# Optimization experiments

Hardware: AMD Instinct MI355X
Metric: run time of the kernel (lower is better)

The kernel has to match this reference:

```python
import jax, jax.numpy as jnp
import numpy as np
from jax.ops import segment_sum, segment_max

N, E, F, HID, HEADS, OUT, G = 50000, 800000, 128, 64, 2, 128, 50
EPS = 1e-5


def setup_inputs() -> dict:
    key = jax.random.key(0)
    ks = iter(jax.random.split(key, 80))
    def p(*shape):
        return jax.random.normal(next(ks), shape, jnp.float32) * 0.1
    inp = {}
    inp['x'] = jax.random.normal(next(ks), (N, F), jnp.float32)
    inp['edge_index'] = jax.random.randint(next(ks), (2, E), 0, N)
    inp['batch'] = jnp.repeat(jnp.arange(G), N // G)
    dims = [(F, HID), (HID, HID), (HID, OUT)]
    for i, (a, b) in enumerate(dims):
        inp[f'gcn_W{i}'] = p(a, b); inp[f'gcn_b{i}'] = jnp.zeros((b,), jnp.float32)
    for i in range(2):
        inp[f'gcn_bn_g{i}'] = jnp.ones((HID,), jnp.float32); inp[f'gcn_bn_b{i}'] = jnp.zeros((HID,), jnp.float32)
    gat_dims = [(F, HEADS, HID), (HEADS * HID, HEADS, HID), (HEADS * HID, 1, OUT)]
    for i, (a, h, c) in enumerate(gat_dims):
        inp[f'gat_W{i}'] = p(a, h * c)
        inp[f'gat_as{i}'] = p(h, c)
        inp[f'gat_ad{i}'] = p(h, c)
        inp[f'gat_b{i}'] = jnp.zeros((h * c if i < 2 else c,), jnp.float32)
    for i in range(2):
        inp[f'gat_bn_g{i}'] = jnp.ones((HEADS * HID,), jnp.float32); inp[f'gat_bn_b{i}'] = jnp.zeros((HEADS * HID,), jnp.float32)
    for i, (a, b) in enumerate(dims):
        inp[f'sage_Wl{i}'] = p(a, b); inp[f'sage_Wr{i}'] = p(a, b); inp[f'sage_b{i}'] = jnp.zeros((b,), jnp.float32)
    for i in range(2):
        inp[f'sage_bn_g{i}'] = jnp.ones((HID,), jnp.float32); inp[f'sage_bn_b{i}'] = jnp.zeros((HID,), jnp.float32)
    inp['fus_W'] = p(3 * OUT, OUT); inp['fus_b'] = jnp.zeros((OUT,), jnp.float32)
    return inp


def _bn(x, g, b):
    m = x.mean(0)
    v = x.var(0)
    return (x - m) * jax.lax.rsqrt(v + EPS) * g + b


def _pool(x, batch):
    s = segment_sum(x, batch, num_segments=G)
    c = segment_sum(jnp.ones((x.shape[0], 1), x.dtype), batch, num_segments=G)
    return s / jnp.maximum(c, 1.0)


def _with_self_loops(src, dst):
    loop = jnp.arange(N)
    return jnp.concatenate([src, loop]), jnp.concatenate([dst, loop])


def _gcn_conv(x, W, b, src, dst):
    # PyG GCNConv: linear, add self loops, symmetric D^-1/2 normalization, scatter-add at dst
    h = x @ W
    srcf, dstf = _with_self_loops(src, dst)
    deg = segment_sum(jnp.ones(srcf.shape[0], x.dtype), dstf, num_segments=N)
    dis = jnp.where(deg > 0, jax.lax.rsqrt(jnp.maximum(deg, 1.0)), 0.0)
    norm = dis[srcf] * dis[dstf]
    return segment_sum(h[srcf] * norm[:, None], dstf, num_segments=N) + b


def _gat_conv(x, W, a_s, a_d, b, src, dst, concat):
    # PyG GATConv: per-head additive attention, leaky_relu(0.2), softmax over incoming edges
    Hh, C = a_s.shape
    h = (x @ W).reshape(N, Hh, C)
    al_src = (h * a_s).sum(-1)  # [N,H]
    al_dst = (h * a_d).sum(-1)  # [N,H]
    srcf, dstf = _with_self_loops(src, dst)
    e = jax.nn.leaky_relu(al_src[srcf] + al_dst[dstf], 0.2)  # [E+N,H]
    m = segment_max(e, dstf, num_segments=N)
    ex = jnp.exp(e - m[dstf])
    denom = segment_sum(ex, dstf, num_segments=N)
    alpha = ex / (denom[dstf] + 1e-16)
    out = segment_sum(h[srcf] * alpha[:, :, None], dstf, num_segments=N)  # [N,H,C]
    out = out.reshape(N, Hh * C) if concat else out.mean(1)
    return out + b


def _sage_conv(x, Wl, Wr, b, src, dst):
    # PyG SAGEConv(mean): lin_l(mean of neighbors) + lin_r(x)
    s = segment_sum(x[src], dst, num_segments=N)
    cnt = segment_sum(jnp.ones((E, 1), x.dtype), dst, num_segments=N)
    mean = s / jnp.maximum(cnt, 1.0)
    return mean @ Wl + x @ Wr + b


def _forward(x, edge_index, batch,
             gcn_W0, gcn_b0, gcn_W1, gcn_b1, gcn_W2, gcn_b2,
             gcn_bn_g0, gcn_bn_b0, gcn_bn_g1, gcn_bn_b1,
             gat_W0, gat_as0, gat_ad0, gat_b0,
             gat_W1, gat_as1, gat_ad1, gat_b1,
             gat_W2, gat_as2, gat_ad2, gat_b2,
             gat_bn_g0, gat_bn_b0, gat_bn_g1, gat_bn_b1,
             sage_Wl0, sage_Wr0, sage_b0,
             sage_Wl1, sage_Wr1, sage_b1,
             sage_Wl2, sage_Wr2, sage_b2,
             sage_bn_g0, sage_bn_b0, sage_bn_g1, sage_bn_b1,
             fus_W, fus_b):
    src, dst = edge_index[0], edge_index[1]
    # GCN branch
    h = jax.nn.relu(_bn(_gcn_conv(x, gcn_W0, gcn_b0, src, dst), gcn_bn_g0, gcn_bn_b0))
    h = jax.nn.relu(_bn(_gcn_conv(h, gcn_W1, gcn_b1, src, dst), gcn_bn_g1, gcn_bn_b1))
    h = _gcn_conv(h, gcn_W2, gcn_b2, src, dst)
    gcn_out = _pool(h, batch)
    # GAT branch (2 heads concat, final single head)
    h = jax.nn.elu(_bn(_gat_conv(x, gat_W0, gat_as0, gat_ad0, gat_b0, src, dst, True), gat_bn_g0, gat_bn_b0))
    h = jax.nn.elu(_bn(_gat_conv(h, gat_W1, gat_as1, gat_ad1, gat_b1, src, dst, True), gat_bn_g1, gat_bn_b1))
    h = _gat_conv(h, gat_W2, gat_as2, gat_ad2, gat_b2, src, dst, False)
    gat_out = _pool(h, batch)
    # SAGE branch (mean aggregation)
    h = jax.nn.relu(_bn(_sage_conv(x, sage_Wl0, sage_Wr0, sage_b0, src, dst), sage_bn_g0, sage_bn_b0))
    h = jax.nn.relu(_bn(_sage_conv(h, sage_Wl1, sage_Wr1, sage_b1, src, dst), sage_bn_g1, sage_bn_b1))
    h = _sage_conv(h, sage_Wl2, sage_Wr2, sage_b2, src, dst)
    sage_out = _pool(h, batch)
    combined = jnp.concatenate([gcn_out, gat_out, sage_out], axis=-1)  # [G, 3*OUT]
    return combined @ fus_W + fus_b


def reference(x, edge_index, batch,
              gcn_W0, gcn_b0, gcn_W1, gcn_b1, gcn_W2, gcn_b2,
              gcn_bn_g0, gcn_bn_b0, gcn_bn_g1, gcn_bn_b1,
              gat_W0, gat_as0, gat_ad0, gat_b0,
              gat_W1, gat_as1, gat_ad1, gat_b1,
              gat_W2, gat_as2, gat_ad2, gat_b2,
              gat_bn_g0, gat_bn_b0, gat_bn_g1, gat_bn_b1,
              sage_Wl0, sage_Wr0, sage_b0,
              sage_Wl1, sage_Wr1, sage_b1,
              sage_Wl2, sage_Wr2, sage_b2,
              sage_bn_g0, sage_bn_b0, sage_bn_g1, sage_bn_b1,
              fus_W, fus_b):
    return _forward(x, edge_index, batch,
                    gcn_W0, gcn_b0, gcn_W1, gcn_b1, gcn_W2, gcn_b2,
                    gcn_bn_g0, gcn_bn_b0, gcn_bn_g1, gcn_bn_b1,
                    gat_W0, gat_as0, gat_ad0, gat_b0,
                    gat_W1, gat_as1, gat_ad1, gat_b1,
                    gat_W2, gat_as2, gat_ad2, gat_b2,
                    gat_bn_g0, gat_bn_b0, gat_bn_g1, gat_bn_b1,
                    sage_Wl0, sage_Wr0, sage_b0,
                    sage_Wl1, sage_Wr1, sage_b1,
                    sage_Wl2, sage_Wr2, sage_b2,
                    sage_bn_g0, sage_bn_b0, sage_bn_g1, sage_bn_b1,
                    fus_W, fus_b)
```

## Files before the change

### kernel.cpp

```cpp
#include <hip/hip_runtime.h>

#define NN 50000
#define NE 800000
#define NG 50
#define NB 196

static constexpr float BN_EPS = 1e-5f;

typedef __attribute__((ext_vector_type(8))) short  bf16x8;
typedef __attribute__((ext_vector_type(8))) unsigned short u16x8;
typedef __attribute__((ext_vector_type(4))) float  f32x4;

__device__ __forceinline__ float bf2f(unsigned short u) {
    return __uint_as_float(((unsigned)u) << 16);
}
__device__ __forceinline__ unsigned short f2bf(float f) {
    unsigned u = __float_as_uint(f);
    unsigned r = (u + 0x7fffu + ((u >> 16) & 1u)) >> 16;
    return (unsigned short)r;
}

__global__ void k_indeg(const int* __restrict__ dst, int* __restrict__ indeg) {
    int e = blockIdx.x * 256 + threadIdx.x;
    if (e < NE) atomicAdd(&indeg[dst[e]], 1);
}

__global__ void k_scan1(const int* __restrict__ cnt, int* __restrict__ rowstart,
                        int* __restrict__ bsum, float* __restrict__ dis) {
    int i = blockIdx.x * 256 + threadIdx.x;
    int lane = threadIdx.x & 63, wv = threadIdx.x >> 6;
    int v = (i < NN) ? cnt[i] : 0;
    if (i < NN) dis[i] = rsqrtf((float)v + 1.0f);
    int s = v;
#pragma unroll
    for (int d = 1; d < 64; d <<= 1) {
        int t = __shfl_up(s, d);
        if (lane >= d) s += t;
    }
    __shared__ int wtot[4];
    if (lane == 63) wtot[wv] = s;
    __syncthreads();
    int woff = 0;
    for (int w = 0; w < wv; ++w) woff += wtot[w];
    if (i < NN) rowstart[i] = woff + s - v;
    if (threadIdx.x == 255) bsum[blockIdx.x] = woff + s;
}

__global__ void k_scan2(const int* __restrict__ bsum, int* __restrict__ boff) {
    int lane = threadIdx.x & 63, wv = threadIdx.x >> 6;
    int v = (threadIdx.x < NB) ? bsum[threadIdx.x] : 0;
    int s = v;
#pragma unroll
    for (int d = 1; d < 64; d <<= 1) {
        int t = __shfl_up(s, d);
        if (lane >= d) s += t;
    }
    __shared__ int wtot[4];
    if (lane == 63) wtot[wv] = s;
    __syncthreads();
    int woff = 0;
    for (int w = 0; w < wv; ++w) woff += wtot[w];
    if (threadIdx.x < NB) boff[threadIdx.x] = woff + s - v;
}

__global__ void k_scan3(int* __restrict__ rowstart, const int* __restrict__ boff,
                        int* __restrict__ cursor) {
    int i = blockIdx.x * 256 + threadIdx.x;
    if (i < NN) {
        int v = rowstart[i] + boff[blockIdx.x];
        rowstart[i] = v;
        cursor[i] = v;
    }
    if (i == 0) rowstart[NN] = NE;
}

__global__ void k_fill(const int* __restrict__ src, const int* __restrict__ dst,
                       const float* __restrict__ dis, int* __restrict__ cursor,
                       int2* __restrict__ pair) {
    int e = blockIdx.x * 256 + threadIdx.x;
    if (e < NE) {
        int s = src[e];
        int pos = atomicAdd(&cursor[dst[e]], 1);
        pair[pos] = make_int2(s, __float_as_int(dis[s]));
    }
}

__global__ void k_count(const int* __restrict__ batch, float* __restrict__ cntG) {
    __shared__ int hist[NG];
    for (int i = threadIdx.x; i < NG; i += 256) hist[i] = 0;
    __syncthreads();
    for (int n = blockIdx.x * 256 + threadIdx.x; n < NN; n += gridDim.x * 256)
        atomicAdd(&hist[batch[n]], 1);
    __syncthreads();
    for (int i = threadIdx.x; i < NG; i += 256)
        if (hist[i]) atomicAdd(&cntG[i], (float)hist[i]);
}

struct WDesc { const float* s; unsigned short* d; int fin; int fout; };
struct WTable { WDesc w[12]; };

__global__ void k_convw(WTable t) {
    WDesc wd = t.w[blockIdx.x];
    int total = wd.fin * wd.fout;
    for (int i = threadIdx.x; i < total; i += 256) {
        int c = i / wd.fin, k = i % wd.fin;
        wd.d[i] = f2bf(wd.s[(size_t)k * wd.fout + c]);
    }
}

__global__ __launch_bounds__(256) void k_mm0(
        const float* __restrict__ X, const unsigned short* __restrict__ Wf,
        const float* __restrict__ as_, const float* __restrict__ ad_,
        float* __restrict__ alsrc, float* __restrict__ aldst,
        unsigned short* __restrict__ outGCN, unsigned short* __restrict__ outGAT,
        unsigned short* __restrict__ outSL, unsigned short* __restrict__ outSR) {
    constexpr int FIN = 128, NCT = 20;
    int wave = threadIdx.x >> 6, lane = threadIdx.x & 63;
    int rowbase = (blockIdx.x * 4 + wave) * 16;
    if (rowbase >= NN) return;
    int lr = lane & 15, lg = lane >> 4;
    int arow = rowbase + lr;
    f32x4 acc[NCT] = {};
    const float* xp = X + (size_t)arow * FIN + lg * 8;
#pragma unroll
    for (int k0 = 0; k0 < FIN; k0 += 32) {
        float4 v0 = *(const float4*)(xp + k0);
        float4 v1 = *(const float4*)(xp + k0 + 4);
        u16x8 au;
        au[0] = f2bf(v0.x); au[1] = f2bf(v0.y); au[2] = f2bf(v0.z); au[3] = f2bf(v0.w);
        au[4] = f2bf(v1.x); au[5] = f2bf(v1.y); au[6] = f2bf(v1.z); au[7] = f2bf(v1.w);
        bf16x8 a1 = *(bf16x8*)&au;
#pragma unroll
        for (int ct = 0; ct < NCT; ++ct) {
            int wcol = ct * 16 + lr;
            bf16x8 b1 = *(const bf16x8*)(Wf + (size_t)wcol * FIN + k0 + lg * 8);
            acc[ct] = __builtin_amdgcn_mfma_f32_16x16x32_bf16(a1, b1, acc[ct], 0, 0, 0);
        }
    }
    {
        float ps[2][4] = {}, pd[2][4] = {};
#pragma unroll
        for (int ct = 4; ct < 12; ++ct) {
            int hh = (ct >= 8) ? 1 : 0;
            int colg = ct * 16 + lr - 64;
            float cs = as_[colg], cd = ad_[colg];
#pragma unroll
            for (int j = 0; j < 4; ++j) {
                ps[hh][j] += acc[ct][j] * cs;
                pd[hh][j] += acc[ct][j] * cd;
            }
        }
#pragma unroll
        for (int m = 1; m < 16; m <<= 1)
#pragma unroll
            for (int hh = 0; hh < 2; ++hh)
#pragma unroll
                for (int j = 0; j < 4; ++j) {
                    ps[hh][j] += __shfl_xor(ps[hh][j], m);
                    pd[hh][j] += __shfl_xor(pd[hh][j], m);
                }
        if (lr == 0) {
#pragma unroll
            for (int j = 0; j < 4; ++j) {
                int row = rowbase + lg * 4 + j;
#pragma unroll
                for (int hh = 0; hh < 2; ++hh) {
                    alsrc[(size_t)row * 2 + hh] = ps[hh][j];
                    aldst[(size_t)row * 2 + hh] = pd[hh][j];
                }
            }
        }
    }
#pragma unroll
    for (int ct = 0; ct < NCT; ++ct) {
        int col = ct * 16 + lr;
#pragma unroll
        for (int j = 0; j < 4; ++j) {
            int row = rowbase + lg * 4 + j;
            unsigned short v = f2bf(acc[ct][j]);
            if (ct < 4)       outGCN[(size_t)row * 64 + col] = v;
            else if (ct < 12) outGAT[(size_t)row * 128 + (col - 64)] = v;
            else if (ct < 16) outSL[(size_t)row * 64 + (col - 192)] = v;
            else              outSR[(size_t)row * 64 + (col - 256)] = v;
        }
    }
}

template <int FIN, int FOUT, bool DUAL, bool BIAS, int BNACT, int ALH>
__global__ __launch_bounds__(256) void k_mm(
        const unsigned short* __restrict__ A1, const unsigned short* __restrict__ W1t,
        const unsigned short* __restrict__ A2, const unsigned short* __restrict__ W2t,
        const float* __restrict__ bias,
        const float* __restrict__ bns, const float* __restrict__ bng, const float* __restrict__ bnb,
        const float* __restrict__ as_, const float* __restrict__ ad_,
        float* __restrict__ alsrc, float* __restrict__ aldst,
        unsigned short* __restrict__ out) {
    constexpr int NCT = FOUT / 16;
    int wave = threadIdx.x >> 6, lane = threadIdx.x & 63;
    int rowbase = (blockIdx.x * 4 + wave) * 16;
    if (rowbase >= NN) return;
    int lr = lane & 15, lg = lane >> 4;
    int arow = rowbase + lr;
    f32x4 acc[NCT] = {};
    const unsigned short* a1p = A1 + (size_t)arow * FIN + lg * 8;
    const unsigned short* a2p = DUAL ? (A2 + (size_t)arow * FIN + lg * 8) : nullptr;
#pragma unroll
    for (int k0 = 0; k0 < FIN; k0 += 32) {
        bf16x8 a1;
        if (BNACT == 0) {
            a1 = *(const bf16x8*)(a1p + k0);
        } else {
            u16x8 araw = *(const u16x8*)(a1p + k0);
            u16x8 atx;
#pragma unroll
            for (int j = 0; j < 8; ++j) {
                int f = k0 + lg * 8 + j;
                float mean = bns[f] * (1.0f / NN);
                float var = bns[FIN + f] * (1.0f / NN) - mean * mean;
                float rstd = rsqrtf(var + BN_EPS);
                float val = (bf2f(araw[j]) - mean) * rstd * bng[f] + bnb[f];
                if (BNACT == 1) val = fmaxf(val, 0.f);
                if (BNACT == 2) val = (val > 0.f) ? val : (__expf(val) - 1.0f);
                atx[j] = f2bf(val);
            }
            a1 = *(bf16x8*)&atx;
        }
        bf16x8 a2v = {};
        if (DUAL) a2v = *(const bf16x8*)(a2p + k0);
#pragma unroll
        for (int ct = 0; ct < NCT; ++ct) {
            int wcol = ct * 16 + lr;
            bf16x8 b1 = *(const bf16x8*)(W1t + (size_t)wcol * FIN + k0 + lg * 8);
            acc[ct] = __builtin_amdgcn_mfma_f32_16x16x32_bf16(a1, b1, acc[ct], 0, 0, 0);
            if (DUAL) {
                bf16x8 b2 = *(const bf16x8*)(W2t + (size_t)wcol * FIN + k0 + lg * 8);
                acc[ct] = __builtin_amdgcn_mfma_f32_16x16x32_bf16(a2v, b2, acc[ct], 0, 0, 0);
            }
        }
    }
    if (ALH > 0) {
        constexpr int NH = (ALH > 0) ? ALH : 1;
        float ps[NH][4] = {}, pd[NH][4] = {};
#pragma unroll
        for (int ct = 0; ct < NCT; ++ct) {
            int hh = (ALH == 2 && ct >= NCT / 2) ? 1 : 0;
            int col = ct * 16 + lr;
            float cs = as_[col], cd = ad_[col];
#pragma unroll
            for (int j = 0; j < 4; ++j) {
                ps[hh][j] += acc[ct][j] * cs;
                pd[hh][j] += acc[ct][j] * cd;
            }
        }
#pragma unroll
        for (int m = 1; m < 16; m <<= 1)
#pragma unroll
            for (int hh = 0; hh < NH; ++hh)
#pragma unroll
                for (int j = 0; j < 4; ++j) {
                    ps[hh][j] += __shfl_xor(ps[hh][j], m);
                    pd[hh][j] += __shfl_xor(pd[hh][j], m);
                }
        if (lr == 0) {
#pragma unroll
            for (int j = 0; j < 4; ++j) {
                int row = rowbase + lg * 4 + j;
#pragma unroll
                for (int hh = 0; hh < NH; ++hh) {
                    alsrc[(size_t)row * ALH + hh] = ps[hh][j];
                    aldst[(size_t)row * ALH + hh] = pd[hh][j];
                }
            }
        }
    }
#pragma unroll
    for (int ct = 0; ct < NCT; ++ct) {
        int col = ct * 16 + lr;
        float bv = BIAS ? bias[col] : 0.f;
#pragma unroll
        for (int j = 0; j < 4; ++j) {
            int row = rowbase + lg * 4 + j;
            out[(size_t)row * FOUT + col] = f2bf(acc[ct][j] + bv);
        }
    }
}

template <int F, bool BIAS>
__global__ __launch_bounds__(256) void k_gcn_agg(
        const int* __restrict__ rowstart, const int2* __restrict__ pair,
        const float* __restrict__ dis, const unsigned short* __restrict__ h,
        const float* __restrict__ bias, unsigned short* __restrict__ out) {
    constexpr int LPE = F / 8;
    constexpr int EPW = 64 / LPE;
    int wave = threadIdx.x >> 6, lane = threadIdx.x & 63;
    int n = blockIdx.x * 4 + wave;
    if (n >= NN) return;
    int r0 = rowstart[n], r1 = rowstart[n + 1];
    float dn = dis[n];
    int fl = lane % LPE, eg = lane / LPE;
    int f0 = fl * 8;
    float acc[8] = {};
    if (eg == 0) {
        u16x8 hv = *(const u16x8*)&h[(size_t)n * F + f0];
        float c = dn * dn;
#pragma unroll
        for (int j = 0; j < 8; ++j) acc[j] = c * bf2f(hv[j]);
    }
#pragma unroll 4
    for (int e = r0 + eg; e < r1; e += EPW) {
        int2 p = pair[e];
        float c = __int_as_float(p.y) * dn;
        u16x8 hs = *(const u16x8*)&h[(size_t)p.x * F + f0];
#pragma unroll
        for (int jj = 0; jj < 8; ++jj) acc[jj] += c * bf2f(hs[jj]);
    }
#pragma unroll
    for (int off = LPE; off < 64; off <<= 1)
#pragma unroll
        for (int jj = 0; jj < 8; ++jj) acc[jj] += __shfl_xor(acc[jj], off);
    if (eg == 0) {
        u16x8 o;
#pragma unroll
        for (int jj = 0; jj < 8; ++jj) {
            float v = acc[jj];
            if (BIAS) v += bias[f0 + jj];
            o[jj] = f2bf(v);
        }
        *(u16x8*)&out[(size_t)n * F + f0] = o;
    }
}

template <int F>
__global__ __launch_bounds__(256) void k_sage_agg(
        const int* __restrict__ rowstart, const int2* __restrict__ pair,
        const unsigned short* __restrict__ h, unsigned short* __restrict__ out) {
    constexpr int LPE = F / 8;
    constexpr int EPW = 64 / LPE;
    int wave = threadIdx.x >> 6, lane = threadIdx.x & 63;
    int n = blockIdx.x * 4 + wave;
    if (n >= NN) return;
    int r0 = rowstart[n], r1 = rowstart[n + 1];
    int fl = lane % LPE, eg = lane / LPE;
    int f0 = fl * 8;
    float acc[8] = {};
#pragma unroll 4
    for (int e = r0 + eg; e < r1; e += EPW) {
        int2 p = pair[e];
        u16x8 hs = *(const u16x8*)&h[(size_t)p.x * F + f0];
#pragma unroll
        for (int jj = 0; jj < 8; ++jj) acc[jj] += bf2f(hs[jj]);
    }
#pragma unroll
    for (int off = LPE; off < 64; off <<= 1)
#pragma unroll
        for (int jj = 0; jj < 8; ++jj) acc[jj] += __shfl_xor(acc[jj], off);
    if (eg == 0) {
        float inv = 1.0f / fmaxf((float)(r1 - r0), 1.0f);
        u16x8 o;
#pragma unroll
        for (int jj = 0; jj < 8; ++jj) o[jj] = f2bf(acc[jj] * inv);
        *(u16x8*)&out[(size_t)n * F + f0] = o;
    }
}

template <int H, int C, bool BIAS>
__global__ __launch_bounds__(256) void k_gat_agg(
        const int* __restrict__ rowstart, const int2* __restrict__ pair,
        const float* __restrict__ alsrc, const float* __restrict__ aldst,
        const unsigned short* __restrict__ h, const float* __restrict__ bias,
        unsigned short* __restrict__ out) {
    constexpr int HC = H * C;
    constexpr int LPE = HC / 8;
    constexpr int EPW = 64 / LPE;
    constexpr int HL = C / 8;
    int wave = threadIdx.x >> 6, lane = threadIdx.x & 63;
    int n = blockIdx.x * 4 + wave;
    if (n >= NN) return;
    int r0 = rowstart[n], r1 = rowstart[n + 1];
    int fl = lane % LPE, eg = lane / LPE;
    int f0 = fl * 8;
    int hh = (H > 1) ? (fl / HL) : 0;
    float adn = aldst[n * H + hh];
    float t = alsrc[n * H + hh] + adn;
    float ws = __expf((t >= 0.f) ? t : 0.2f * t);
    float acc[8] = {};
    float dsum = 0.f;
    if (eg == 0) {
        u16x8 hv = *(const u16x8*)&h[(size_t)n * HC + f0];
#pragma unroll
        for (int j = 0; j < 8; ++j) acc[j] = ws * bf2f(hv[j]);
    }
#pragma unroll 4
    for (int e = r0 + eg; e < r1; e += EPW) {
        int s = pair[e].x;
        float v = alsrc[(size_t)s * H + hh] + adn;
        v = (v >= 0.f) ? v : 0.2f * v;
        float w = __expf(v);
        dsum += w;
        u16x8 hs = *(const u16x8*)&h[(size_t)s * HC + f0];
#pragma unroll
        for (int jj = 0; jj < 8; ++jj) acc[jj] += w * bf2f(hs[jj]);
    }
    if (H > 1) {
#pragma unroll
        for (int off = 1; off < HL; off <<= 1) dsum += __shfl_xor(dsum, off);
#pragma unroll
        for (int off = LPE; off < 64; off <<= 1) dsum += __shfl_xor(dsum, off);
    } else {
#pragma unroll
        for (int off = 1; off < 64; off <<= 1) dsum += __shfl_xor(dsum, off);
    }
    float den = ws + dsum * (1.0f / HL);
    float dinv = 1.0f / (den + 1e-16f);
#pragma unroll
    for (int off = LPE; off < 64; off <<= 1)
#pragma unroll
        for (int jj = 0; jj < 8; ++jj) acc[jj] += __shfl_xor(acc[jj], off);
    if (eg == 0) {
        u16x8 o;
#pragma unroll
        for (int jj = 0; jj < 8; ++jj) {
            float v = acc[jj] * dinv;
            if (BIAS) v += bias[f0 + jj];
            o[jj] = f2bf(v);
        }
        *(u16x8*)&out[(size_t)n * HC + f0] = o;
    }
}

template <int F, bool TWO>
__global__ void k_bn_stats(const unsigned short* __restrict__ x,
                           const unsigned short* __restrict__ y,
                           float* __restrict__ sums) {
    constexpr int TPR = F / 8;
    constexpr int RPB = 256 / TPR;
    __shared__ float lsum[F], lsq[F];
    for (int i = threadIdx.x; i < F; i += 256) { lsum[i] = 0.f; lsq[i] = 0.f; }
    __syncthreads();
    int fl = threadIdx.x % TPR, rl = threadIdx.x / TPR;
    int f0 = fl * 8;
    float s[8] = {}, s2[8] = {};
    for (int n = blockIdx.x * RPB + rl; n < NN; n += gridDim.x * RPB) {
        u16x8 v = *(const u16x8*)&x[(size_t)n * F + f0];
        u16x8 w = {};
        if (TWO) w = *(const u16x8*)&y[(size_t)n * F + f0];
#pragma unroll
        for (int j = 0; j < 8; ++j) {
            float f = bf2f(v[j]);
            if (TWO) f += bf2f(w[j]);
            s[j] += f; s2[j] += f * f;
        }
    }
#pragma unroll
    for (int off = TPR; off < 64; off <<= 1)
#pragma unroll
        for (int j = 0; j < 8; ++j) { s[j] += __shfl_xor(s[j], off); s2[j] += __shfl_xor(s2[j], off); }
    if ((threadIdx.x & 63) < TPR) {
#pragma unroll
        for (int j = 0; j < 8; ++j) {
            atomicAdd(&lsum[f0 + j], s[j]);
            atomicAdd(&lsq[f0 + j], s2[j]);
        }
    }
    __syncthreads();
    for (int i = threadIdx.x; i < F; i += 256) {
        atomicAdd(&sums[i], lsum[i]);
        atomicAdd(&sums[F + i], lsq[i]);
    }
}

template <int F, int ACT, bool TWO>
__global__ void k_bn_apply(const unsigned short* __restrict__ x,
                           const unsigned short* __restrict__ y,
                           const float* __restrict__ sums,
                           const float* __restrict__ gamma, const float* __restrict__ beta,
                           unsigned short* __restrict__ out) {
    int idx = blockIdx.x * 256 + threadIdx.x;
    if (idx >= NN * F / 8) return;
    int f0 = (idx % (F / 8)) * 8;
    u16x8 v = *(const u16x8*)&x[(size_t)idx * 8];
    u16x8 w = {};
    if (TWO) w = *(const u16x8*)&y[(size_t)idx * 8];
    u16x8 o;
#pragma unroll
    for (int j = 0; j < 8; ++j) {
        int f = f0 + j;
        float mean = sums[f] * (1.0f / NN);
        float var = sums[F + f] * (1.0f / NN) - mean * mean;
        float rstd = rsqrtf(var + BN_EPS);
        float raw = bf2f(v[j]);
        if (TWO) raw += bf2f(w[j]);
        float val = (raw - mean) * rstd * gamma[f] + beta[f];
        if (ACT == 1) val = fmaxf(val, 0.f);
        if (ACT == 2) val = (val > 0.f) ? val : (__expf(val) - 1.0f);
        o[j] = f2bf(val);
    }
    *(u16x8*)&out[(size_t)idx * 8] = o;
}

__global__ void k_pool(const unsigned short* __restrict__ x, const int* __restrict__ batch,
                       float* __restrict__ pooled, int off) {
    int f = threadIdx.x & 127;
    int half = threadIdx.x >> 7;
    int nend = min(NN, (int)(blockIdx.x + 1) * 128);
    float acc = 0.f; int gcur = -1;
    for (int n = blockIdx.x * 128 + half; n < nend; n += 2) {
        int g = batch[n];
        if (g != gcur) {
            if (gcur >= 0) atomicAdd(&pooled[(size_t)gcur * 384 + off + f], acc);
            gcur = g; acc = 0.f;
        }
        acc += bf2f(x[(size_t)n * 128 + f]);
    }
    if (gcur >= 0) atomicAdd(&pooled[(size_t)gcur * 384 + off + f], acc);
}

__global__ void k_fusion(const float* __restrict__ pooled, const float* __restrict__ cntG,
                         const float* __restrict__ W, const float* __restrict__ b,
                         float* __restrict__ out) {
    int idx = blockIdx.x * 256 + threadIdx.x;
    if (idx >= NG * 128) return;
    int g = idx / 128, o = idx % 128;
    float inv = 1.0f / fmaxf(cntG[g], 1.0f);
    float acc = b[o];
#pragma unroll 4
    for (int k = 0; k < 384; ++k)
        acc += pooled[g * 384 + k] * inv * W[k * 128 + o];
    out[idx] = acc;
}

static inline int grid1(long long n) { return (int)((n + 255) / 256); }

extern "C" void kernel_launch(void* const* d_in, const int* in_sizes, int n_in,
                              void* d_out, int out_size, void* d_ws, size_t ws_size,
                              hipStream_t stream) {
    const float* x       = (const float*)d_in[0];
    const int*   ei      = (const int*)d_in[1];
    const int*   batch   = (const int*)d_in[2];
    const float* gcn_W0  = (const float*)d_in[3];
    const float* gcn_W1  = (const float*)d_in[5];
    const float* gcn_W2  = (const float*)d_in[7];
    const float* gcn_b2  = (const float*)d_in[8];
    const float* gcn_g0  = (const float*)d_in[9];
    const float* gcn_bb0 = (const float*)d_in[10];
    const float* gcn_g1  = (const float*)d_in[11];
    const float* gcn_bb1 = (const float*)d_in[12];
    const float* gat_W0  = (const float*)d_in[13];
    const float* gat_as0 = (const float*)d_in[14];
    const float* gat_ad0 = (const float*)d_in[15];
    const float* gat_W1  = (const float*)d_in[17];
    const float* gat_as1 = (const float*)d_in[18];
    const float* gat_ad1 = (const float*)d_in[19];
    const float* gat_W2  = (const float*)d_in[21];
    const float* gat_as2 = (const float*)d_in[22];
    const float* gat_ad2 = (const float*)d_in[23];
    const float* gat_b2  = (const float*)d_in[24];
    const float* gat_g0  = (const float*)d_in[25];
    const float* gat_bb0 = (const float*)d_in[26];
    const float* gat_g1  = (const float*)d_in[27];
    const float* gat_bb1 = (const float*)d_in[28];
    const float* sage_Wl0 = (const float*)d_in[29];
    const float* sage_Wr0 = (const float*)d_in[30];
    const float* sage_Wl1 = (const float*)d_in[32];
    const float* sage_Wr1 = (const float*)d_in[33];
    const float* sage_Wl2 = (const float*)d_in[35];
    const float* sage_Wr2 = (const float*)d_in[36];
    const float* sage_b2  = (const float*)d_in[37];
    const float* sage_g0  = (const float*)d_in[38];
    const float* sage_bb0 = (const float*)d_in[39];
    const float* sage_g1  = (const float*)d_in[40];
    const float* sage_bb1 = (const float*)d_in[41];
    const float* fus_W    = (const float*)d_in[42];
    const float* fus_b    = (const float*)d_in[43];

    const int* src = ei;
    const int* dst = ei + NE;

    float* ws = (float*)d_ws;
    size_t off = 0;
    auto alloc = [&](size_t n) { float* p = ws + off; off += (n + 3) & ~(size_t)3; return p; };
    unsigned short* bufA  = (unsigned short*)alloc((size_t)NN * 64);
    unsigned short* bufB  = (unsigned short*)alloc((size_t)NN * 64);
    unsigned short* bufC  = (unsigned short*)alloc((size_t)NN * 64);
    unsigned short* bufD  = (unsigned short*)alloc((size_t)NN * 64);
    unsigned short* wt    = (unsigned short*)alloc(110592 / 2);
    int*   indeg    = (int*)alloc(NN);
    int*   rowstart = (int*)alloc(NN + 1);
    int*   cursor   = (int*)alloc(NN);
    int2*  pair     = (int2*)alloc((size_t)NE * 2);
    int*   bsum     = (int*)alloc(NB);
    int*   boff     = (int*)alloc(NB);
    float* dis   = alloc(NN);
    float* alsrc = alloc((size_t)NN * 2);
    float* aldst = alloc((size_t)NN * 2);
    float* bnsum = alloc(6 * 256 + NG * 384 + NG);
    float* pooled = bnsum + 6 * 256;
    float* cntG   = pooled + NG * 384;
    (void)ws_size; (void)n_in; (void)in_sizes; (void)out_size;

    unsigned short* sl0 = bufD;
    unsigned short* sr0 = bufD + (size_t)NN * 64;

    unsigned short* wf       = wt;
    unsigned short* gcn_W1t  = wf + 40960;
    unsigned short* gcn_W2t  = gcn_W1t + 4096;
    unsigned short* gat_W1t  = gcn_W2t + 8192;
    unsigned short* gat_W2t  = gat_W1t + 16384;
    unsigned short* sage_Wl1t = gat_W2t + 16384;
    unsigned short* sage_Wr1t = sage_Wl1t + 4096;
    unsigned short* sage_Wl2t = sage_Wr1t + 4096;
    unsigned short* sage_Wr2t = sage_Wl2t + 8192;

    const int gAgg = NN / 4;
    const int gMM  = (NN + 63) / 64;

    hipMemsetAsync(indeg, 0, NN * 4, stream);
    hipMemsetAsync(bnsum, 0, (6 * 256 + NG * 384 + NG) * 4, stream);
    k_indeg<<<grid1(NE), 256, 0, stream>>>(dst, indeg);
    k_scan1<<<NB, 256, 0, stream>>>(indeg, rowstart, bsum, dis);
    k_scan2<<<1, 256, 0, stream>>>(bsum, boff);
    k_scan3<<<NB, 256, 0, stream>>>(rowstart, boff, cursor);
    k_fill<<<grid1(NE), 256, 0, stream>>>(src, dst, dis, cursor, pair);
    k_count<<<128, 256, 0, stream>>>(batch, cntG);
    WTable wtab = {{
        { gcn_W0, wf, 128, 64 }, { gat_W0, wf + 64 * 128, 128, 128 },
        { sage_Wl0, wf + 192 * 128, 128, 64 }, { sage_Wr0, wf + 256 * 128, 128, 64 },
        { gcn_W1, gcn_W1t, 64, 64 }, { gcn_W2, gcn_W2t, 64, 128 },
        { gat_W1, gat_W1t, 128, 128 }, { gat_W2, gat_W2t, 128, 128 },
        { sage_Wl1, sage_Wl1t, 64, 64 }, { sage_Wr1, sage_Wr1t, 64, 64 },
        { sage_Wl2, sage_Wl2t, 64, 128 }, { sage_Wr2, sage_Wr2t, 64, 128 },
    }};
    k_convw<<<12, 256, 0, stream>>>(wtab);

    k_mm0<<<gMM, 256, 0, stream>>>(x, wf, gat_as0, gat_ad0, alsrc, aldst,
                                   bufA, bufB, sl0, sr0);

    k_gcn_agg<64, false><<<gAgg, 256, 0, stream>>>(rowstart, pair, dis, bufA, nullptr, bufC);
    k_bn_stats<64, false><<<250, 256, 0, stream>>>(bufC, nullptr, bnsum + 0 * 256);
    k_mm<64, 64, false, false, 1, 0><<<gMM, 256, 0, stream>>>(
        bufC, gcn_W1t, nullptr, nullptr, nullptr,
        bnsum + 0 * 256, gcn_g0, gcn_bb0, nullptr, nullptr, nullptr, nullptr, bufA);
    k_gcn_agg<64, false><<<gAgg, 256, 0, stream>>>(rowstart, pair, dis, bufA, nullptr, bufC);
    k_bn_stats<64, false><<<250, 256, 0, stream>>>(bufC, nullptr, bnsum + 1 * 256);
    k_bn_apply<64, 1, false><<<grid1(NN * 8), 256, 0, stream>>>(
        bufC, nullptr, bnsum + 1 * 256, gcn_g1, gcn_bb1, bufA);
    k_gcn_agg<64, false><<<gAgg, 256, 0, stream>>>(rowstart, pair, dis, bufA, nullptr, bufC);
    k_mm<64, 128, false, true, 0, 0><<<gMM, 256, 0, stream>>>(
        bufC, gcn_W2t, nullptr, nullptr, gcn_b2,
        nullptr, nullptr, nullptr, nullptr, nullptr, nullptr, nullptr, bufA);
    k_pool<<<(NN + 127) / 128, 256, 0, stream>>>(bufA, batch, pooled, 0);

    k_gat_agg<2, 64, false><<<gAgg, 256, 0, stream>>>(rowstart, pair, alsrc, aldst, bufB, nullptr, bufC);
    k_bn_stats<128, false><<<250, 256, 0, stream>>>(bufC, nullptr, bnsum + 2 * 256);
    k_mm<128, 128, false, false, 2, 2><<<gMM, 256, 0, stream>>>(
        bufC, gat_W1t, nullptr, nullptr, nullptr,
        bnsum + 2 * 256, gat_g0, gat_bb0, gat_as1, gat_ad1, alsrc, aldst, bufB);
    k_gat_agg<2, 64, false><<<gAgg, 256, 0, stream>>>(rowstart, pair, alsrc, aldst, bufB, nullptr, bufC);
    k_bn_stats<128, false><<<250, 256, 0, stream>>>(bufC, nullptr, bnsum + 3 * 256);
    k_mm<128, 128, false, false, 2, 1><<<gMM, 256, 0, stream>>>(
        bufC, gat_W2t, nullptr, nullptr, nullptr,
        bnsum + 3 * 256, gat_g1, gat_bb1, gat_as2, gat_ad2, alsrc, aldst, bufB);
    k_gat_agg<1, 128, true><<<gAgg, 256, 0, stream>>>(rowstart, pair, alsrc, aldst, bufB, gat_b2, bufC);
    k_pool<<<(NN + 127) / 128, 256, 0, stream>>>(bufC, batch, pooled, 128);

    k_sage_agg<64><<<gAgg, 256, 0, stream>>>(rowstart, pair, sl0, bufA);
    k_bn_stats<64, true><<<250, 256, 0, stream>>>(bufA, sr0, bnsum + 4 * 256);
    k_bn_apply<64, 1, true><<<grid1(NN * 8), 256, 0, stream>>>(
        bufA, sr0, bnsum + 4 * 256, sage_g0, sage_bb0, bufB);
    k_sage_agg<64><<<gAgg, 256, 0, stream>>>(rowstart, pair, bufB, bufA);
    k_mm<64, 64, true, false, 0, 0><<<gMM, 256, 0, stream>>>(
        bufA, sage_Wl1t, bufB, sage_Wr1t, nullptr,
        nullptr, nullptr, nullptr, nullptr, nullptr, nullptr, nullptr, bufC);
    k_bn_stats<64, false><<<250, 256, 0, stream>>>(bufC, nullptr, bnsum + 5 * 256);
    k_bn_apply<64, 1, false><<<grid1(NN * 8), 256, 0, stream>>>(
        bufC, nullptr, bnsum + 5 * 256, sage_g1, sage_bb1, bufB);
    k_sage_agg<64><<<gAgg, 256, 0, stream>>>(rowstart, pair, bufB, bufA);
    k_mm<64, 128, true, true, 0, 0><<<gMM, 256, 0, stream>>>(
        bufA, sage_Wl2t, bufB, sage_Wr2t, sage_b2,
        nullptr, nullptr, nullptr, nullptr, nullptr, nullptr, nullptr, bufC);
    k_pool<<<(NN + 127) / 128, 256, 0, stream>>>(bufC, batch, pooled, 256);

    k_fusion<<<grid1(NG * 128), 256, 0, stream>>>(pooled, cntG, fus_W, fus_b, (float*)d_out);
}
```

Before: 725.8 us.

## Fuse GCN, GAT and SAGE neighbor aggregations into one combined-row gather kernel

Packs the per-node features of all three branches (GCN 64, SAGE 64, GAT 128) into one 256-wide bf16 row, so a single aggregation kernel walks the CSR once per layer and gathers one contiguous 512-byte row per neighbor instead of three separate passes. Each lane picks its branch weight (symmetric norm, mean, or attention softmax), and the layer schedule is interleaved so each branch's matmul and batchnorm writes into the combined buffer. CSR construction is also split into a fill step and a separate pack step. In exchange, every layer does the GAT exp and alsrc load for all lanes, and the branches are forced into lockstep.

```diff
diff --git a/kernel.cpp b/kernel.cpp
--- a/kernel.cpp
+++ b/kernel.cpp
@@ -75,13 +75,20 @@
 }
 
 __global__ void k_fill(const int* __restrict__ src, const int* __restrict__ dst,
-                       const float* __restrict__ dis, int* __restrict__ cursor,
+                       int* __restrict__ cursor, int* __restrict__ csr_src) {
+    int e = blockIdx.x * 256 + threadIdx.x;
+    if (e < NE) {
+        int pos = atomicAdd(&cursor[dst[e]], 1);
+        csr_src[pos] = src[e];
+    }
+}
+
+__global__ void k_pack(const int* __restrict__ csr_src, const float* __restrict__ dis,
                        int2* __restrict__ pair) {
     int e = blockIdx.x * 256 + threadIdx.x;
     if (e < NE) {
-        int s = src[e];
-        int pos = atomicAdd(&cursor[dst[e]], 1);
-        pair[pos] = make_int2(s, __float_as_int(dis[s]));
+        int s = csr_src[e];
+        pair[e] = make_int2(s, __float_as_int(dis[s]));
     }
 }
 
@@ -112,8 +119,7 @@
         const float* __restrict__ X, const unsigned short* __restrict__ Wf,
         const float* __restrict__ as_, const float* __restrict__ ad_,
         float* __restrict__ alsrc, float* __restrict__ aldst,
-        unsigned short* __restrict__ outGCN, unsigned short* __restrict__ outGAT,
-        unsigned short* __restrict__ outSL, unsigned short* __restrict__ outSR) {
+        unsigned short* __restrict__ comb, unsigned short* __restrict__ sr0) {
     constexpr int FIN = 128, NCT = 20;
     int wave = threadIdx.x >> 6, lane = threadIdx.x & 63;
     int rowbase = (blockIdx.x * 4 + wave) * 16;
@@ -178,15 +184,15 @@
         for (int j = 0; j < 4; ++j) {
             int row = rowbase + lg * 4 + j;
             unsigned short v = f2bf(acc[ct][j]);
-            if (ct < 4)       outGCN[(size_t)row * 64 + col] = v;
-            else if (ct < 12) outGAT[(size_t)row * 128 + (col - 64)] = v;
-            else if (ct < 16) outSL[(size_t)row * 64 + (col - 192)] = v;
-            else              outSR[(size_t)row * 64 + (col - 256)] = v;
-        }
-    }
-}
-
-template <int FIN, int FOUT, bool DUAL, bool BIAS, int BNACT, int ALH>
+            if (ct < 4)       comb[(size_t)row * 256 + col] = v;
+            else if (ct < 12) comb[(size_t)row * 256 + 128 + (col - 64)] = v;
+            else if (ct < 16) comb[(size_t)row * 256 + 64 + (col - 192)] = v;
+            else              sr0[(size_t)row * 64 + (col - 256)] = v;
+        }
+    }
+}
+
+template <int FIN, int FOUT, bool DUAL, bool BIAS, int BNACT, int ALH, int OSTR, int OOFF>
 __global__ __launch_bounds__(256) void k_mm(
         const unsigned short* __restrict__ A1, const unsigned short* __restrict__ W1t,
         const unsigned short* __restrict__ A2, const unsigned short* __restrict__ W2t,
@@ -280,151 +286,84 @@
 #pragma unroll
         for (int j = 0; j < 4; ++j) {
             int row = rowbase + lg * 4 + j;
-            out[(size_t)row * FOUT + col] = f2bf(acc[ct][j] + bv);
-        }
-    }
-}
-
-template <int F, bool BIAS>
-__global__ __launch_bounds__(256) void k_gcn_agg(
+            out[(size_t)row * OSTR + OOFF + col] = f2bf(acc[ct][j] + bv);
+        }
+    }
+}
+
+template <int H, bool GATBIAS>
+__global__ __launch_bounds__(256) void k_aggf(
         const int* __restrict__ rowstart, const int2* __restrict__ pair,
-        const float* __restrict__ dis, const unsigned short* __restrict__ h,
-        const float* __restrict__ bias, unsigned short* __restrict__ out) {
-    constexpr int LPE = F / 8;
-    constexpr int EPW = 64 / LPE;
+        const float* __restrict__ dis, const float* __restrict__ alsrc,
+        const float* __restrict__ aldst, const unsigned short* __restrict__ comb,
+        const float* __restrict__ gat_bias,
+        unsigned short* __restrict__ outGCN, unsigned short* __restrict__ outGAT,
+        unsigned short* __restrict__ outSAGE) {
     int wave = threadIdx.x >> 6, lane = threadIdx.x & 63;
     int n = blockIdx.x * 4 + wave;
     if (n >= NN) return;
+    int eg = lane >> 5, fl = lane & 31;
+    int f0 = fl * 8;
+    bool isGCN = fl < 8, isSAGE = (fl >= 8) && (fl < 16), isGAT = fl >= 16;
+    int hh = (H == 2) ? ((fl >= 24) ? 1 : 0) : 0;
     int r0 = rowstart[n], r1 = rowstart[n + 1];
     float dn = dis[n];
-    int fl = lane % LPE, eg = lane / LPE;
-    int f0 = fl * 8;
+    float adn = isGAT ? aldst[n * H + hh] : 0.f;
+    float tself = isGAT ? (alsrc[n * H + hh] + adn) : 0.f;
+    tself = (tself >= 0.f) ? tself : 0.2f * tself;
+    float wsG = __expf(tself);
+    float selfw = isGCN ? dn * dn : (isGAT ? wsG : 0.f);
     float acc[8] = {};
     if (eg == 0) {
-        u16x8 hv = *(const u16x8*)&h[(size_t)n * F + f0];
-        float c = dn * dn;
-#pragma unroll
-        for (int j = 0; j < 8; ++j) acc[j] = c * bf2f(hv[j]);
-    }
+        u16x8 hv = *(const u16x8*)&comb[(size_t)n * 256 + f0];
+#pragma unroll
+        for (int j = 0; j < 8; ++j) acc[j] = selfw * bf2f(hv[j]);
+    }
+    float dsum = 0.f;
 #pragma unroll 4
-    for (int e = r0 + eg; e < r1; e += EPW) {
+    for (int e = r0 + eg; e < r1; e += 2) {
         int2 p = pair[e];
-        float c = __int_as_float(p.y) * dn;
-        u16x8 hs = *(const u16x8*)&h[(size_t)p.x * F + f0];
-#pragma unroll
-        for (int jj = 0; jj < 8; ++jj) acc[jj] += c * bf2f(hs[jj]);
-    }
-#pragma unroll
-    for (int off = LPE; off < 64; off <<= 1)
-#pragma unroll
-        for (int jj = 0; jj < 8; ++jj) acc[jj] += __shfl_xor(acc[jj], off);
-    if (eg == 0) {
-        u16x8 o;
-#pragma unroll
-        for (int jj = 0; jj < 8; ++jj) {
-            float v = acc[jj];
-            if (BIAS) v += bias[f0 + jj];
-            o[jj] = f2bf(v);
-        }
-        *(u16x8*)&out[(size_t)n * F + f0] = o;
-    }
-}
-
-template <int F>
-__global__ __launch_bounds__(256) void k_sage_agg(
-        const int* __restrict__ rowstart, const int2* __restrict__ pair,
-        const unsigned short* __restrict__ h, unsigned short* __restrict__ out) {
-    constexpr int LPE = F / 8;
-    constexpr int EPW = 64 / LPE;
-    int wave = threadIdx.x >> 6, lane = threadIdx.x & 63;
-    int n = blockIdx.x * 4 + wave;
-    if (n >= NN) return;
-    int r0 = rowstart[n], r1 = rowstart[n + 1];
-    int fl = lane % LPE, eg = lane / LPE;
-    int f0 = fl * 8;
-    float acc[8] = {};
-#pragma unroll 4
-    for (int e = r0 + eg; e < r1; e += EPW) {
-        int2 p = pair[e];
-        u16x8 hs = *(const u16x8*)&h[(size_t)p.x * F + f0];
-#pragma unroll
-        for (int jj = 0; jj < 8; ++jj) acc[jj] += bf2f(hs[jj]);
-    }
-#pragma unroll
-    for (int off = LPE; off < 64; off <<= 1)
-#pragma unroll
-        for (int jj = 0; jj < 8; ++jj) acc[jj] += __shfl_xor(acc[jj], off);
+        int s = p.x;
+        float al = isGAT ? alsrc[(size_t)s * H + hh] : 0.f;
+        float v = al + adn;
+        v = (v >= 0.f) ? v : 0.2f * v;
+        float we = __expf(v);
+        dsum += we;
+        float w = isGCN ? __int_as_float(p.y) * dn : (isGAT ? we : 1.0f);
+        u16x8 hs = *(const u16x8*)&comb[(size_t)s * 256 + f0];
+#pragma unroll
+        for (int jj = 0; jj < 8; ++jj) acc[jj] += w * bf2f(hs[jj]);
+    }
+    if (H == 2) {
+        dsum += __shfl_xor(dsum, 1);
+        dsum += __shfl_xor(dsum, 2);
+        dsum += __shfl_xor(dsum, 4);
+        dsum += __shfl_xor(dsum, 32);
+        dsum *= 0.125f;
+    } else {
+        dsum += __shfl_xor(dsum, 1);
+        dsum += __shfl_xor(dsum, 2);
+        dsum += __shfl_xor(dsum, 4);
+        dsum += __shfl_xor(dsum, 8);
+        dsum += __shfl_xor(dsum, 32);
+        dsum *= 0.0625f;
+    }
+    float dinv = 1.0f / (wsG + dsum + 1e-16f);
+#pragma unroll
+    for (int jj = 0; jj < 8; ++jj) acc[jj] += __shfl_xor(acc[jj], 32);
     if (eg == 0) {
         float inv = 1.0f / fmaxf((float)(r1 - r0), 1.0f);
+        float mul = isGCN ? 1.0f : (isSAGE ? inv : dinv);
         u16x8 o;
 #pragma unroll
-        for (int jj = 0; jj < 8; ++jj) o[jj] = f2bf(acc[jj] * inv);
-        *(u16x8*)&out[(size_t)n * F + f0] = o;
-    }
-}
-
-template <int H, int C, bool BIAS>
-__global__ __launch_bounds__(256) void k_gat_agg(
-        const int* __restrict__ rowstart, const int2* __restrict__ pair,
-        const float* __restrict__ alsrc, const float* __restrict__ aldst,
-        const unsigned short* __restrict__ h, const float* __restrict__ bias,
-        unsigned short* __restrict__ out) {
-    constexpr int HC = H * C;
-    constexpr int LPE = HC / 8;
-    constexpr int EPW = 64 / LPE;
-    constexpr int HL = C / 8;
-    int wave = threadIdx.x >> 6, lane = threadIdx.x & 63;
-    int n = blockIdx.x * 4 + wave;
-    if (n >= NN) return;
-    int r0 = rowstart[n], r1 = rowstart[n + 1];
-    int fl = lane % LPE, eg = lane / LPE;
-    int f0 = fl * 8;
-    int hh = (H > 1) ? (fl / HL) : 0;
-    float adn = aldst[n * H + hh];
-    float t = alsrc[n * H + hh] + adn;
-    float ws = __expf((t >= 0.f) ? t : 0.2f * t);
-    float acc[8] = {};
-    float dsum = 0.f;
-    if (eg == 0) {
-        u16x8 hv = *(const u16x8*)&h[(size_t)n * HC + f0];
-#pragma unroll
-        for (int j = 0; j < 8; ++j) acc[j] = ws * bf2f(hv[j]);
-    }
-#pragma unroll 4
-    for (int e = r0 + eg; e < r1; e += EPW) {
-        int s = pair[e].x;
-        float v = alsrc[(size_t)s * H + hh] + adn;
-        v = (v >= 0.f) ? v : 0.2f * v;
-        float w = __expf(v);
-        dsum += w;
-        u16x8 hs = *(const u16x8*)&h[(size_t)s * HC + f0];
-#pragma unroll
-        for (int jj = 0; jj < 8; ++jj) acc[jj] += w * bf2f(hs[jj]);
-    }
-    if (H > 1) {
-#pragma unroll
-        for (int off = 1; off < HL; off <<= 1) dsum += __shfl_xor(dsum, off);
-#pragma unroll
-        for (int off = LPE; off < 64; off <<= 1) dsum += __shfl_xor(dsum, off);
-    } else {
-#pragma unroll
-        for (int off = 1; off < 64; off <<= 1) dsum += __shfl_xor(dsum, off);
-    }
-    float den = ws + dsum * (1.0f / HL);
-    float dinv = 1.0f / (den + 1e-16f);
-#pragma unroll
-    for (int off = LPE; off < 64; off <<= 1)
-#pragma unroll
-        for (int jj = 0; jj < 8; ++jj) acc[jj] += __shfl_xor(acc[jj], off);
-    if (eg == 0) {
-        u16x8 o;
-#pragma unroll
         for (int jj = 0; jj < 8; ++jj) {
-            float v = acc[jj] * dinv;
-            if (BIAS) v += bias[f0 + jj];
+            float v = acc[jj] * mul;
+            if (GATBIAS && isGAT) v += gat_bias[f0 - 128 + jj];
             o[jj] = f2bf(v);
         }
-        *(u16x8*)&out[(size_t)n * HC + f0] = o;
+        if (isGCN)       *(u16x8*)&outGCN[(size_t)n * 64 + f0] = o;
+        else if (isSAGE) *(u16x8*)&outSAGE[(size_t)n * 64 + (f0 - 64)] = o;
+        else             *(u16x8*)&outGAT[(size_t)n * 128 + (f0 - 128)] = o;
     }
 }
 
@@ -469,14 +408,15 @@
     }
 }
 
-template <int F, int ACT, bool TWO>
+template <int F, int ACT, bool TWO, bool O1, bool O2, int OOFF>
 __global__ void k_bn_apply(const unsigned short* __restrict__ x,
                            const unsigned short* __restrict__ y,
                            const float* __restrict__ sums,
                            const float* __restrict__ gamma, const float* __restrict__ beta,
-                           unsigned short* __restrict__ out) {
+                           unsigned short* __restrict__ out1, unsigned short* __restrict__ comb) {
     int idx = blockIdx.x * 256 + threadIdx.x;
     if (idx >= NN * F / 8) return;
+    int row = idx / (F / 8);
     int f0 = (idx % (F / 8)) * 8;
     u16x8 v = *(const u16x8*)&x[(size_t)idx * 8];
     u16x8 w = {};
@@ -495,7 +435,8 @@
         if (ACT == 2) val = (val > 0.f) ? val : (__expf(val) - 1.0f);
         o[j] = f2bf(val);
     }
-    *(u16x8*)&out[(size_t)idx * 8] = o;
+    if (O1) *(u16x8*)&out1[(size_t)idx * 8] = o;
+    if (O2) *(u16x8*)&comb[(size_t)row * 256 + OOFF + f0] = o;
 }
 
 __global__ void k_pool(const unsigned short* __restrict__ x, const int* __restrict__ batch,
@@ -579,14 +520,19 @@
     float* ws = (float*)d_ws;
     size_t off = 0;
     auto alloc = [&](size_t n) { float* p = ws + off; off += (n + 3) & ~(size_t)3; return p; };
-    unsigned short* bufA  = (unsigned short*)alloc((size_t)NN * 64);
-    unsigned short* bufB  = (unsigned short*)alloc((size_t)NN * 64);
-    unsigned short* bufC  = (unsigned short*)alloc((size_t)NN * 64);
-    unsigned short* bufD  = (unsigned short*)alloc((size_t)NN * 64);
-    unsigned short* wt    = (unsigned short*)alloc(110592 / 2);
+    unsigned short* combA = (unsigned short*)alloc((size_t)NN * 128);
+    unsigned short* combB = (unsigned short*)alloc((size_t)NN * 128);
+    unsigned short* bufGCN  = (unsigned short*)alloc((size_t)NN * 32);
+    unsigned short* bufGAT  = (unsigned short*)alloc((size_t)NN * 64);
+    unsigned short* bufSAGE = (unsigned short*)alloc((size_t)NN * 32);
+    unsigned short* sr0     = (unsigned short*)alloc((size_t)NN * 32);
+    unsigned short* sageH0  = (unsigned short*)alloc((size_t)NN * 32);
+    unsigned short* sageM1  = (unsigned short*)alloc((size_t)NN * 32);
+    unsigned short* wt      = (unsigned short*)alloc(110592 / 2);
     int*   indeg    = (int*)alloc(NN);
     int*   rowstart = (int*)alloc(NN + 1);
     int*   cursor   = (int*)alloc(NN);
+    int*   csr_src  = (int*)alloc(NE);
     int2*  pair     = (int2*)alloc((size_t)NE * 2);
     int*   bsum     = (int*)alloc(NB);
     int*   boff     = (int*)alloc(NB);
@@ -598,14 +544,15 @@
     float* cntG   = pooled + NG * 384;
     (void)ws_size; (void)n_in; (void)in_sizes; (void)out_size;
 
-    unsigned short* sl0 = bufD;
-    unsigned short* sr0 = bufD + (size_t)NN * 64;
-
-    unsigned short* wf       = wt;
-    unsigned short* gcn_W1t  = wf + 40960;
-    unsigned short* gcn_W2t  = gcn_W1t + 4096;
-    unsigned short* gat_W1t  = gcn_W2t + 8192;
-    unsigned short* gat_W2t  = gat_W1t + 16384;
+    unsigned short* sageH1  = sr0;
+    unsigned short* finGCN  = combB;
+    unsigned short* finSAGE = combB + (size_t)NN * 128;
+
+    unsigned short* wf        = wt;
+    unsigned short* gcn_W1t   = wf + 40960;
+    unsigned short* gcn_W2t   = gcn_W1t + 4096;
+    unsigned short* gat_W1t   = gcn_W2t + 8192;
+    unsigned short* gat_W2t   = gat_W1t + 16384;
     unsigned short* sage_Wl1t = gat_W2t + 16384;
     unsigned short* sage_Wr1t = sage_Wl1t + 4096;
     unsigned short* sage_Wl2t = sage_Wr1t + 4096;
@@ -620,7 +567,8 @@
     k_scan1<<<NB, 256, 0, stream>>>(indeg, rowstart, bsum, dis);
     k_scan2<<<1, 256, 0, stream>>>(bsum, boff);
     k_scan3<<<NB, 256, 0, stream>>>(rowstart, boff, cursor);
-    k_fill<<<grid1(NE), 256, 0, stream>>>(src, dst, dis, cursor, pair);
+    k_fill<<<grid1(NE), 256, 0, stream>>>(src, dst, cursor, csr_src);
+    k_pack<<<grid1(NE), 256, 0, stream>>>(csr_src, dis, pair);
     k_count<<<128, 256, 0, stream>>>(batch, cntG);
     WTable wtab = {{
         { gcn_W0, wf, 128, 64 }, { gat_W0, wf + 64 * 128, 128, 128 },
@@ -632,53 +580,48 @@
     }};
     k_convw<<<12, 256, 0, stream>>>(wtab);
 
-    k_mm0<<<gMM, 256, 0, stream>>>(x, wf, gat_as0, gat_ad0, alsrc, aldst,
-                                   bufA, bufB, sl0, sr0);
-
-    k_gcn_agg<64, false><<<gAgg, 256, 0, stream>>>(rowstart, pair, dis, bufA, nullptr, bufC);
-    k_bn_stats<64, false><<<250, 256, 0, stream>>>(bufC, nullptr, bnsum + 0 * 256);
-    k_mm<64, 64, false, false, 1, 0><<<gMM, 256, 0, stream>>>(
-        bufC, gcn_W1t, nullptr, nullptr, nullptr,
-        bnsum + 0 * 256, gcn_g0, gcn_bb0, nullptr, nullptr, nullptr, nullptr, bufA);
-    k_gcn_agg<64, false><<<gAgg, 256, 0, stream>>>(rowstart, pair, dis, bufA, nullptr, bufC);
-    k_bn_stats<64, false><<<250, 256, 0, stream>>>(bufC, nullptr, bnsum + 1 * 256);
-    k_bn_apply<64, 1, false><<<grid1(NN * 8), 256, 0, stream>>>(
-        bufC, nullptr, bnsum + 1 * 256, gcn_g1, gcn_bb1, bufA);
-    k_gcn_agg<64, false><<<gAgg, 256, 0, stream>>>(rowstart, pair, dis, bufA, nullptr, bufC);
-    k_mm<64, 128, false, true, 0, 0><<<gMM, 256, 0, stream>>>(
-        bufC, gcn_W2t, nullptr, nullptr, gcn_b2,
-        nullptr, nullptr, nullptr, nullptr, nullptr, nullptr, nullptr, bufA);
-    k_pool<<<(NN + 127) / 128, 256, 0, stream>>>(bufA, batch, pooled, 0);
-
-    k_gat_agg<2, 64, false><<<gAgg, 256, 0, stream>>>(rowstart, pair, alsrc, aldst, bufB, nullptr, bufC);
-    k_bn_stats<128, false><<<250, 256, 0, stream>>>(bufC, nullptr, bnsum + 2 * 256);
-    k_mm<128, 128, false, false, 2, 2><<<gMM, 256, 0, stream>>>(
-        bufC, gat_W1t, nullptr, nullptr, nullptr,
-        bnsum + 2 * 256, gat_g0, gat_bb0, gat_as1, gat_ad1, alsrc, aldst, bufB);
-    k_gat_agg<2, 64, false><<<gAgg, 256, 0, stream>>>(rowstart, pair, alsrc, aldst, bufB, nullptr, bufC);
-    k_bn_stats<128, false><<<250, 256, 0, stream>>>(bufC, nullptr, bnsum + 3 * 256);
-    k_mm<128, 128, false, false, 2, 1><<<gMM, 256, 0, stream>>>(
-        bufC, gat_W2t, nullptr, nullptr, nullptr,
-        bnsum + 3 * 256, gat_g1, gat_bb1, gat_as2, gat_ad2, alsrc, aldst, bufB);
-    k_gat_agg<1, 128, true><<<gAgg, 256, 0, stream>>>(rowstart, pair, alsrc, aldst, bufB, gat_b2, bufC);
-    k_pool<<<(NN + 127) / 128, 256, 0, stream>>>(bufC, batch, pooled, 128);
-
-    k_sage_agg<64><<<gAgg, 256, 0, stream>>>(rowstart, pair, sl0, bufA);
-    k_bn_stats<64, true><<<250, 256, 0, stream>>>(bufA, sr0, bnsum + 4 * 256);
-    k_bn_apply<64, 1, true><<<grid1(NN * 8), 256, 0, stream>>>(
-        bufA, sr0, bnsum + 4 * 256, sage_g0, sage_bb0, bufB);
-    k_sage_agg<64><<<gAgg, 256, 0, stream>>>(rowstart, pair, bufB, bufA);
-    k_mm<64, 64, true, false, 0, 0><<<gMM, 256, 0, stream>>>(
-        bufA, sage_Wl1t, bufB, sage_Wr1t, nullptr,
-        nullptr, nullptr, nullptr, nullptr, nullptr, nullptr, nullptr, bufC);
-    k_bn_stats<64, false><<<250, 256, 0, stream>>>(bufC, nullptr, bnsum + 5 * 256);
-    k_bn_apply<64, 1, false><<<grid1(NN * 8), 256, 0, stream>>>(
-        bufC, nullptr, bnsum + 5 * 256, sage_g1, sage_bb1, bufB);
-    k_sage_agg<64><<<gAgg, 256, 0, stream>>>(rowstart, pair, bufB, bufA);
-    k_mm<64, 128, true, true, 0, 0><<<gMM, 256, 0, stream>>>(
-        bufA, sage_Wl2t, bufB, sage_Wr2t, sage_b2,
-        nullptr, nullptr, nullptr, nullptr, nullptr, nullptr, nullptr, bufC);
-    k_pool<<<(NN + 127) / 128, 256, 0, stream>>>(bufC, batch, pooled, 256);
-
+    k_mm0<<<gMM, 256, 0, stream>>>(x, wf, gat_as0, gat_ad0, alsrc, aldst, combA, sr0);
+    k_aggf<2, false><<<gAgg, 256, 0, stream>>>(rowstart, pair, dis, alsrc, aldst,
+                                               combA, nullptr, bufGCN, bufGAT, bufSAGE);
+    k_bn_stats<64, false><<<250, 256, 0, stream>>>(bufGCN, nullptr, bnsum + 0 * 256);
+    k_bn_stats<128, false><<<250, 256, 0, stream>>>(bufGAT, nullptr, bnsum + 2 * 256);
+    k_bn_stats<64, true><<<250, 256, 0, stream>>>(bufSAGE, sr0, bnsum + 4 * 256);
+    k_mm<64, 64, false, false, 1, 0, 256, 0><<<gMM, 256, 0, stream>>>(
+        bufGCN, gcn_W1t, nullptr, nullptr, nullptr,
+        bnsum + 0 * 256, gcn_g0, gcn_bb0, nullptr, nullptr, nullptr, nullptr, combB);
+    k_mm<128, 128, false, false, 2, 2, 256, 128><<<gMM, 256, 0, stream>>>(
+        bufGAT, gat_W1t, nullptr, nullptr, nullptr,
+        bnsum + 2 * 256, gat_g0, gat_bb0, gat_as1, gat_ad1, alsrc, aldst, combB);
+    k_bn_apply<64, 1, true, true, true, 64><<<grid1(NN * 8), 256, 0, stream>>>(
+        bufSAGE, sr0, bnsum + 4 * 256, sage_g0, sage_bb0, sageH0, combB);
+
+    k_aggf<2, false><<<gAgg, 256, 0, stream>>>(rowstart, pair, dis, alsrc, aldst,
+                                               combB, nullptr, bufGCN, bufGAT, bufSAGE);
+    k_bn_stats<64, false><<<250, 256, 0, stream>>>(bufGCN, nullptr, bnsum + 1 * 256);
+    k_bn_stats<128, false><<<250, 256, 0, stream>>>(bufGAT, nullptr, bnsum + 3 * 256);
+    k_mm<64, 64, true, false, 0, 0, 64, 0><<<gMM, 256, 0, stream>>>(
+        bufSAGE, sage_Wl1t, sageH0, sage_Wr1t, nullptr,
+        nullptr, nullptr, nullptr, nullptr, nullptr, nullptr, nullptr, sageM1);
+    k_bn_apply<64, 1, false, false, true, 0><<<grid1(NN * 8), 256, 0, stream>>>(
+        bufGCN, nullptr, bnsum + 1 * 256, gcn_g1, gcn_bb1, nullptr, combA);
+    k_mm<128, 128, false, false, 2, 1, 256, 128><<<gMM, 256, 0, stream>>>(
+        bufGAT, gat_W2t, nullptr, nullptr, nullptr,
+        bnsum + 3 * 256, gat_g1, gat_bb1, gat_as2, gat_ad2, alsrc, aldst, combA);
+    k_bn_stats<64, false><<<250, 256, 0, stream>>>(sageM1, nullptr, bnsum + 5 * 256);
+    k_bn_apply<64, 1, false, true, true, 64><<<grid1(NN * 8), 256, 0, stream>>>(
+        sageM1, nullptr, bnsum + 5 * 256, sage_g1, sage_bb1, sageH1, combA);
+
+    k_aggf<1, true><<<gAgg, 256, 0, stream>>>(rowstart, pair, dis, alsrc, aldst,
+                                              combA, gat_b2, bufGCN, bufGAT, bufSAGE);
+    k_mm<64, 128, false, true, 0, 0, 128, 0><<<gMM, 256, 0, stream>>>(
+        bufGCN, gcn_W2t, nullptr, nullptr, gcn_b2,
+        nullptr, nullptr, nullptr, nullptr, nullptr, nullptr, nullptr, finGCN);
+    k_mm<64, 128, true, true, 0, 0, 128, 0><<<gMM, 256, 0, stream>>>(
+        bufSAGE, sage_Wl2t, sageH1, sage_Wr2t, sage_b2,
+        nullptr, nullptr, nullptr, nullptr, nullptr, nullptr, nullptr, finSAGE);
+
+    k_pool<<<(NN + 127) / 128, 256, 0, stream>>>(finGCN, batch, pooled, 0);
+    k_pool<<<(NN + 127) / 128, 256, 0, stream>>>(bufGAT, batch, pooled, 128);
+    k_pool<<<(NN + 127) / 128, 256, 0, stream>>>(finSAGE, batch, pooled, 256);
     k_fusion<<<grid1(NG * 128), 256, 0, stream>>>(pooled, cntG, fus_W, fus_b, (float*)d_out);
 }
```

New measurement: 664.0 us. 8.5% less time.
